# Kernel optimization log

Measured on AMD Instinct MI355X. Metric: run time of the kernel, lower is better.

Reference implementation:

```python
import jax, jax.numpy as jnp
import numpy as np

E = 1024          # n_embed_dim
H = 64            # head_size = n_embed_dim // n_heads (16)

def setup_inputs() -> dict:
    key = jax.random.key(0)
    k_x, k_q, k_k, k_v = jax.random.split(key, 4)
    scale = 1.0 / np.sqrt(E)
    return {
        "x": jax.random.normal(k_x, (4, 2048, E), dtype=jnp.float32),
        "ln_gamma": jnp.ones((E,), jnp.float32),
        "ln_beta": jnp.zeros((E,), jnp.float32),
        # torch nn.Linear weights: [out_features, in_features]
        "Wq": jax.random.normal(k_q, (H, E), dtype=jnp.float32) * scale,
        "Wk": jax.random.normal(k_k, (H, E), dtype=jnp.float32) * scale,
        "Wv": jax.random.normal(k_v, (H, E), dtype=jnp.float32) * scale,
    }

def reference(x, ln_gamma, ln_beta, Wq, Wk, Wv):
    # LayerNorm over last dim (eps matches torch default 1e-5)
    mu = jnp.mean(x, axis=-1, keepdims=True)
    var = jnp.mean(jnp.square(x - mu), axis=-1, keepdims=True)
    xn = (x - mu) * jax.lax.rsqrt(var + 1e-5) * ln_gamma + ln_beta

    q = jnp.einsum('bse,he->bsh', xn, Wq)   # [B,S,H]
    k = jnp.einsum('bse,he->bsh', xn, Wk)
    v = jnp.einsum('bse,he->bsh', xn, Wv)

    scores = jnp.einsum('bqh,bkh->bqk', q, k) / jnp.sqrt(jnp.float32(H))
    S = x.shape[1]
    causal = jnp.tril(jnp.ones((S, S), dtype=bool))
    scores = jnp.where(causal, scores, -jnp.inf)
    attn = jax.nn.softmax(scores, axis=-1)
    return jnp.einsum('bqk,bkh->bqh', attn, v)
```

## Files before the change

kernel.cpp:

```cpp
#include <hip/hip_runtime.h>

#define E 1024
#define HH 64
#define BB 4
#define SS 2048
#define BS (BB*SS)
#define NSLOT 144

typedef unsigned short u16;
typedef short bf16x8 __attribute__((ext_vector_type(8)));
typedef float f32x4 __attribute__((ext_vector_type(4)));

#define LOG2E_O8 0.18033688011112042f

__device__ inline u16 f2bf(float f) {
    unsigned int u = __float_as_uint(f);
    unsigned int r = (u + 0x7FFFu + ((u >> 16) & 1u)) >> 16;
    return (u16)r;
}

__global__ __launch_bounds__(256) void ln_kernel(const float* __restrict__ x,
        const float* __restrict__ gamma, const float* __restrict__ beta,
        u16* __restrict__ xn) {
    const int w = threadIdx.x >> 6, lane = threadIdx.x & 63;
    const size_t row = (size_t)blockIdx.x * 4 + w;
    const float4* xr = (const float4*)(x + row * E);
    float4 v[4];
    #pragma unroll
    for (int i = 0; i < 4; ++i) v[i] = xr[lane + 64 * i];
    float s = 0.f, sq = 0.f;
    #pragma unroll
    for (int i = 0; i < 4; ++i) {
        s  += v[i].x + v[i].y + v[i].z + v[i].w;
        sq += v[i].x*v[i].x + v[i].y*v[i].y + v[i].z*v[i].z + v[i].w*v[i].w;
    }
    #pragma unroll
    for (int off = 32; off > 0; off >>= 1) {
        s  += __shfl_xor(s,  off);
        sq += __shfl_xor(sq, off);
    }
    const float mean = s * (1.0f / E);
    const float var  = sq * (1.0f / E) - mean * mean;
    const float rstd = rsqrtf(var + 1e-5f);
    const float4* gr = (const float4*)gamma;
    const float4* br = (const float4*)beta;
    #pragma unroll
    for (int i = 0; i < 4; ++i) {
        const float4 g  = gr[lane + 64 * i];
        const float4 bt = br[lane + 64 * i];
        ushort4 o;
        o.x = f2bf((v[i].x - mean) * rstd * g.x + bt.x);
        o.y = f2bf((v[i].y - mean) * rstd * g.y + bt.y);
        o.z = f2bf((v[i].z - mean) * rstd * g.z + bt.z);
        o.w = f2bf((v[i].w - mean) * rstd * g.w + bt.w);
        *(ushort4*)(xn + row * E + (lane + 64 * i) * 4) = o;
    }
}

__global__ __launch_bounds__(256) void w_cast(const float* __restrict__ Wq,
        const float* __restrict__ Wk, const float* __restrict__ Wv,
        u16* __restrict__ wc) {
    const int row = blockIdx.x;
    const int t = threadIdx.x;
    const float* src = (row < 64)  ? (Wq + (size_t)row * E)
                     : (row < 128) ? (Wk + (size_t)(row - 64) * E)
                                   : (Wv + (size_t)(row - 128) * E);
    const float sc = (row < 64) ? LOG2E_O8 : 1.0f;
    const float4 v = *(const float4*)(src + t * 4);
    ushort4 o;
    o.x = f2bf(v.x * sc); o.y = f2bf(v.y * sc);
    o.z = f2bf(v.z * sc); o.w = f2bf(v.w * sc);
    *(ushort4*)(wc + (size_t)row * E + t * 4) = o;
}

__global__ __launch_bounds__(256) void qkv_mfma(const u16* __restrict__ xn,
        const u16* __restrict__ wc,
        u16* __restrict__ qb, u16* __restrict__ kb, u16* __restrict__ vt) {
    const int row0 = blockIdx.x * 32;
    const int t = threadIdx.x;
    const int w = t >> 6, lane = t & 63;
    const int quad = lane >> 4, r15 = lane & 15;
    __shared__ u16 Xs[32 * 64];
    __shared__ u16 Ws[192 * 64];
    f32x4 acc[2][3] = {};

    for (int kc = 0; kc < E; kc += 64) {
        __syncthreads();
        {
            const int row = t >> 3, ch = t & 7;
            const uint4 d = *(const uint4*)(xn + (size_t)(row0 + row) * E + kc + ch * 8);
            *(uint4*)&Xs[row * 64 + (ch ^ (row & 7)) * 8] = d;
        }
        #pragma unroll
        for (int i = 0; i < 6; ++i) {
            const int idx = i * 256 + t;
            const int wrow = idx >> 3, ch = idx & 7;
            const uint4 d = *(const uint4*)(wc + (size_t)wrow * E + kc + ch * 8);
            *(uint4*)&Ws[wrow * 64 + (ch ^ (wrow & 7)) * 8] = d;
        }
        __syncthreads();
        #pragma unroll
        for (int kk = 0; kk < 2; ++kk) {
            bf16x8 af[2];
            #pragma unroll
            for (int mt = 0; mt < 2; ++mt) {
                const int xrow = mt * 16 + r15;
                af[mt] = *(const bf16x8*)&Xs[xrow * 64 + ((kk * 4 + quad) ^ (xrow & 7)) * 8];
            }
            #pragma unroll
            for (int j = 0; j < 3; ++j) {
                const int wrow = (w * 3 + j) * 16 + r15;
                const bf16x8 bfr = *(const bf16x8*)&Ws[wrow * 64 + ((kk * 4 + quad) ^ (wrow & 7)) * 8];
                #pragma unroll
                for (int mt = 0; mt < 2; ++mt)
                    acc[mt][j] = __builtin_amdgcn_mfma_f32_16x16x32_bf16(af[mt], bfr, acc[mt][j], 0, 0, 0);
            }
        }
    }
    const int b    = row0 >> 11;
    const int key0 = row0 & 2047;
    #pragma unroll
    for (int mt = 0; mt < 2; ++mt)
        #pragma unroll
        for (int j = 0; j < 3; ++j) {
            const int cg  = w * 48 + j * 16 + r15;
            const int sel = cg >> 6;
            const int col = cg & 63;
            if (sel < 2) {
                u16* base = (sel == 0) ? qb : kb;
                #pragma unroll
                for (int r = 0; r < 4; ++r) {
                    const size_t row = (size_t)row0 + mt * 16 + quad * 4 + r;
                    base[row * HH + col] = f2bf(acc[mt][j][r]);
                }
            } else {
                ushort4 pk;
                pk.x = f2bf(acc[mt][j][0]); pk.y = f2bf(acc[mt][j][1]);
                pk.z = f2bf(acc[mt][j][2]); pk.w = f2bf(acc[mt][j][3]);
                *(ushort4*)(vt + (size_t)b * HH * SS + (size_t)col * SS
                               + key0 + mt * 16 + quad * 4) = pk;
            }
        }
}

__global__ __launch_bounds__(256) void attn_partial(const u16* __restrict__ qb,
        const u16* __restrict__ kb, const u16* __restrict__ vt,
        float* __restrict__ po, float* __restrict__ pm, float* __restrict__ pl) {
    const int bid = blockIdx.x;
    const int b   = bid >> 8;
    const int rem = bid & 255;
    const int qt  = rem >> 3, c = rem & 7;
    const int a   = qt >> 2;
    if (c > a) return;
    const int r_   = qt & 3;
    const int slot = b * NSLOT + 2 * a * (a + 1) + r_ * (a + 1) + c;
    const int q0   = qt << 6;
    const int t = threadIdx.x;
    const int w = t >> 6, lane = t & 63;
    const int quad = lane >> 4, r15 = lane & 15;

    __shared__ u16 Ks[64 * 64];
    __shared__ u16 VT[64 * 64];
    __shared__ u16 Ps[64 * 64];

    const size_t qrow = ((size_t)b * SS + q0 + w * 16 + r15) * HH;
    const bf16x8 qf0 = *(const bf16x8*)(qb + qrow + quad * 8);
    const bf16x8 qf1 = *(const bf16x8*)(qb + qrow + 32 + quad * 8);

    f32x4 o[4] = {};
    float m_[4], l_[4];
    #pragma unroll
    for (int r = 0; r < 4; ++r) { m_[r] = -INFINITY; l_[r] = 0.f; }

    const int t1 = min(c * 4 + 4, qt + 1);
    for (int tile = c * 4; tile < t1; ++tile) {
        const int kt = tile << 6;
        __syncthreads();
        {
            const int row = t >> 2, ch0 = (t & 3) * 2;
            const uint4* src = (const uint4*)(kb + ((size_t)b * SS + kt + row) * HH + ch0 * 8);
            const uint4 d0 = src[0], d1 = src[1];
            *(uint4*)&Ks[row * 64 + ((ch0    ) ^ (row & 7)) * 8] = d0;
            *(uint4*)&Ks[row * 64 + ((ch0 + 1) ^ (row & 7)) * 8] = d1;
        }
        {
            const int h = t >> 2, ch0 = (t & 3) * 2;
            const uint4* src = (const uint4*)(vt + (size_t)b * HH * SS + (size_t)h * SS + kt + ch0 * 8);
            const uint4 d0 = src[0], d1 = src[1];
            *(uint4*)&VT[h * 64 + ((ch0    ) ^ (h & 7)) * 8] = d0;
            *(uint4*)&VT[h * 64 + ((ch0 + 1) ^ (h & 7)) * 8] = d1;
        }
        __syncthreads();

        f32x4 s[4] = {};
        #pragma unroll
        for (int nt = 0; nt < 4; ++nt) {
            const int krow = nt * 16 + r15;
            const bf16x8 k0 = *(const bf16x8*)&Ks[krow * 64 + ((    quad) ^ (krow & 7)) * 8];
            const bf16x8 k1 = *(const bf16x8*)&Ks[krow * 64 + ((4 + quad) ^ (krow & 7)) * 8];
            s[nt] = __builtin_amdgcn_mfma_f32_16x16x32_bf16(qf0, k0, s[nt], 0, 0, 0);
            s[nt] = __builtin_amdgcn_mfma_f32_16x16x32_bf16(qf1, k1, s[nt], 0, 0, 0);
        }
        if (tile == qt) {
            #pragma unroll
            for (int nt = 0; nt < 4; ++nt)
                #pragma unroll
                for (int r = 0; r < 4; ++r)
                    if (nt * 16 + r15 > w * 16 + quad * 4 + r) s[nt][r] = -INFINITY;
        }

        float p[4][4];
        #pragma unroll
        for (int r = 0; r < 4; ++r) {
            float mx = fmaxf(fmaxf(s[0][r], s[1][r]), fmaxf(s[2][r], s[3][r]));
            mx = fmaxf(mx, __shfl_xor(mx, 1));
            mx = fmaxf(mx, __shfl_xor(mx, 2));
            mx = fmaxf(mx, __shfl_xor(mx, 4));
            mx = fmaxf(mx, __shfl_xor(mx, 8));
            const float mn = fmaxf(m_[r], mx);
            const float alpha = __builtin_amdgcn_exp2f(m_[r] - mn);
            m_[r] = mn;
            float rs = 0.f;
            #pragma unroll
            for (int nt = 0; nt < 4; ++nt) {
                p[nt][r] = __builtin_amdgcn_exp2f(s[nt][r] - mn);
                rs += p[nt][r];
            }
            rs += __shfl_xor(rs, 1); rs += __shfl_xor(rs, 2);
            rs += __shfl_xor(rs, 4); rs += __shfl_xor(rs, 8);
            l_[r] = l_[r] * alpha + rs;
            #pragma unroll
            for (int ht = 0; ht < 4; ++ht) o[ht][r] *= alpha;
        }

        #pragma unroll
        for (int nt = 0; nt < 4; ++nt)
            #pragma unroll
            for (int r = 0; r < 4; ++r) {
                const int prow = w * 16 + quad * 4 + r;
                const int col  = nt * 16 + r15;
                Ps[prow * 64 + (((col >> 3) ^ (prow & 7)) * 8) + (col & 7)] = f2bf(p[nt][r]);
            }
        const int arow = w * 16 + r15;
        const bf16x8 pf0 = *(const bf16x8*)&Ps[arow * 64 + ((    quad) ^ (arow & 7)) * 8];
        const bf16x8 pf1 = *(const bf16x8*)&Ps[arow * 64 + ((4 + quad) ^ (arow & 7)) * 8];

        #pragma unroll
        for (int ht = 0; ht < 4; ++ht) {
            const int vrow = ht * 16 + r15;
            const bf16x8 v0 = *(const bf16x8*)&VT[vrow * 64 + ((    quad) ^ (vrow & 7)) * 8];
            const bf16x8 v1 = *(const bf16x8*)&VT[vrow * 64 + ((4 + quad) ^ (vrow & 7)) * 8];
            o[ht] = __builtin_amdgcn_mfma_f32_16x16x32_bf16(pf0, v0, o[ht], 0, 0, 0);
            o[ht] = __builtin_amdgcn_mfma_f32_16x16x32_bf16(pf1, v1, o[ht], 0, 0, 0);
        }
    }

    #pragma unroll
    for (int r = 0; r < 4; ++r) {
        const int q = w * 16 + quad * 4 + r;
        #pragma unroll
        for (int ht = 0; ht < 4; ++ht)
            po[(size_t)slot * 4096 + q * 64 + ht * 16 + r15] = o[ht][r];
        if (r15 == 0) {
            pm[slot * 64 + q] = m_[r];
            pl[slot * 64 + q] = l_[r];
        }
    }
}

__global__ __launch_bounds__(256) void attn_reduce(const float* __restrict__ po,
        const float* __restrict__ pm, const float* __restrict__ pl,
        float* __restrict__ out) {
    const int bid = blockIdx.x;
    const int b = bid >> 7, rem = bid & 127;
    const int qt = rem >> 2, qq = rem & 3;
    const int a = qt >> 2, r_ = qt & 3;
    const int nc = a + 1;
    const int sbase = b * NSLOT + 2 * a * (a + 1) + r_ * (a + 1);
    const int t = threadIdx.x;
    const int h = t & 63, qr = t >> 6;
    #pragma unroll
    for (int i = 0; i < 4; ++i) {
        const int q = qq * 16 + qr * 4 + i;
        float mstar = -INFINITY;
        for (int cidx = 0; cidx < nc; ++cidx)
            mstar = fmaxf(mstar, pm[(sbase + cidx) * 64 + q]);
        float osum = 0.f, lsum = 0.f;
        for (int cidx = 0; cidx < nc; ++cidx) {
            const float sc = __builtin_amdgcn_exp2f(pm[(sbase + cidx) * 64 + q] - mstar);
            osum += sc * po[(size_t)(sbase + cidx) * 4096 + q * 64 + h];
            lsum += sc * pl[(sbase + cidx) * 64 + q];
        }
        out[((size_t)b * SS + (qt << 6) + q) * HH + h] = osum / lsum;
    }
}

extern "C" void kernel_launch(void* const* d_in, const int* in_sizes, int n_in,
                              void* d_out, int out_size, void* d_ws, size_t ws_size,
                              hipStream_t stream) {
    const float* x     = (const float*)d_in[0];
    const float* gamma = (const float*)d_in[1];
    const float* beta  = (const float*)d_in[2];
    const float* Wq    = (const float*)d_in[3];
    const float* Wk    = (const float*)d_in[4];
    const float* Wv    = (const float*)d_in[5];
    float* out = (float*)d_out;

    u16* xn = (u16*)d_ws;
    u16* wc = (u16*)((char*)d_ws + (size_t)BS * E * 2);
    u16* qb = (u16*)((char*)d_ws + (size_t)BS * E * 2 + 393216);
    u16* kb = qb + (size_t)BS * HH;
    u16* vt = kb + (size_t)BS * HH;
    float* po = (float*)d_ws;
    float* pm = po + (size_t)BB * NSLOT * 4096;
    float* pl = pm + (size_t)BB * NSLOT * 64;

    ln_kernel   <<<BS / 4,     256, 0, stream>>>(x, gamma, beta, xn);
    w_cast      <<<192,        256, 0, stream>>>(Wq, Wk, Wv, wc);
    qkv_mfma    <<<BS / 32,    256, 0, stream>>>(xn, wc, qb, kb, vt);
    attn_partial<<<BB * 32 * 8, 256, 0, stream>>>(qb, kb, vt, po, pm, pl);
    attn_reduce <<<BB * 32 * 4, 256, 0, stream>>>(po, pm, pl, out);
}
```

Before: 144.2 us.

## Fuse LayerNorm into QKV projection by folding gamma/beta into weights and bias

Result: slower. 175.7 us (+21.9%).

```diff
diff --git a/kernel.cpp b/kernel.cpp
--- a/kernel.cpp
+++ b/kernel.cpp
@@ -19,47 +19,10 @@
     return (u16)r;
 }
 
-__global__ __launch_bounds__(256) void ln_kernel(const float* __restrict__ x,
-        const float* __restrict__ gamma, const float* __restrict__ beta,
-        u16* __restrict__ xn) {
-    const int w = threadIdx.x >> 6, lane = threadIdx.x & 63;
-    const size_t row = (size_t)blockIdx.x * 4 + w;
-    const float4* xr = (const float4*)(x + row * E);
-    float4 v[4];
-    #pragma unroll
-    for (int i = 0; i < 4; ++i) v[i] = xr[lane + 64 * i];
-    float s = 0.f, sq = 0.f;
-    #pragma unroll
-    for (int i = 0; i < 4; ++i) {
-        s  += v[i].x + v[i].y + v[i].z + v[i].w;
-        sq += v[i].x*v[i].x + v[i].y*v[i].y + v[i].z*v[i].z + v[i].w*v[i].w;
-    }
-    #pragma unroll
-    for (int off = 32; off > 0; off >>= 1) {
-        s  += __shfl_xor(s,  off);
-        sq += __shfl_xor(sq, off);
-    }
-    const float mean = s * (1.0f / E);
-    const float var  = sq * (1.0f / E) - mean * mean;
-    const float rstd = rsqrtf(var + 1e-5f);
-    const float4* gr = (const float4*)gamma;
-    const float4* br = (const float4*)beta;
-    #pragma unroll
-    for (int i = 0; i < 4; ++i) {
-        const float4 g  = gr[lane + 64 * i];
-        const float4 bt = br[lane + 64 * i];
-        ushort4 o;
-        o.x = f2bf((v[i].x - mean) * rstd * g.x + bt.x);
-        o.y = f2bf((v[i].y - mean) * rstd * g.y + bt.y);
-        o.z = f2bf((v[i].z - mean) * rstd * g.z + bt.z);
-        o.w = f2bf((v[i].w - mean) * rstd * g.w + bt.w);
-        *(ushort4*)(xn + row * E + (lane + 64 * i) * 4) = o;
-    }
-}
-
 __global__ __launch_bounds__(256) void w_cast(const float* __restrict__ Wq,
         const float* __restrict__ Wk, const float* __restrict__ Wv,
-        u16* __restrict__ wc) {
+        const float* __restrict__ gamma, const float* __restrict__ beta,
+        u16* __restrict__ wc, float* __restrict__ bias) {
     const int row = blockIdx.x;
     const int t = threadIdx.x;
     const float* src = (row < 64)  ? (Wq + (size_t)row * E)
@@ -67,30 +30,65 @@
                                    : (Wv + (size_t)(row - 128) * E);
     const float sc = (row < 64) ? LOG2E_O8 : 1.0f;
     const float4 v = *(const float4*)(src + t * 4);
+    const float4 g = *(const float4*)(gamma + t * 4);
+    const float4 b = *(const float4*)(beta + t * 4);
     ushort4 o;
-    o.x = f2bf(v.x * sc); o.y = f2bf(v.y * sc);
-    o.z = f2bf(v.z * sc); o.w = f2bf(v.w * sc);
+    o.x = f2bf(v.x * g.x * sc); o.y = f2bf(v.y * g.y * sc);
+    o.z = f2bf(v.z * g.z * sc); o.w = f2bf(v.w * g.w * sc);
     *(ushort4*)(wc + (size_t)row * E + t * 4) = o;
-}
-
-__global__ __launch_bounds__(256) void qkv_mfma(const u16* __restrict__ xn,
-        const u16* __restrict__ wc,
+
+    float s = (v.x * b.x + v.y * b.y + v.z * b.z + v.w * b.w) * sc;
+    #pragma unroll
+    for (int off = 32; off > 0; off >>= 1) s += __shfl_xor(s, off);
+    __shared__ float red[4];
+    if ((t & 63) == 0) red[t >> 6] = s;
+    __syncthreads();
+    if (t == 0) bias[row] = red[0] + red[1] + red[2] + red[3];
+}
+
+__global__ __launch_bounds__(256) void lnqkv(const float* __restrict__ x,
+        const u16* __restrict__ wc, const float* __restrict__ bias,
         u16* __restrict__ qb, u16* __restrict__ kb, u16* __restrict__ vt) {
     const int row0 = blockIdx.x * 32;
     const int t = threadIdx.x;
     const int w = t >> 6, lane = t & 63;
     const int quad = lane >> 4, r15 = lane & 15;
-    __shared__ u16 Xs[32 * 64];
     __shared__ u16 Ws[192 * 64];
+    __shared__ float smu[32], srs[32];
+
+    #pragma unroll 2
+    for (int i = 0; i < 8; ++i) {
+        const int r = w * 8 + i;
+        const float4* xr = (const float4*)(x + (size_t)(row0 + r) * E);
+        float s = 0.f, sq = 0.f;
+        #pragma unroll
+        for (int jj = 0; jj < 4; ++jj) {
+            const float4 v = xr[lane + 64 * jj];
+            s  += v.x + v.y + v.z + v.w;
+            sq += v.x*v.x + v.y*v.y + v.z*v.z + v.w*v.w;
+        }
+        #pragma unroll
+        for (int off = 32; off > 0; off >>= 1) {
+            s  += __shfl_xor(s,  off);
+            sq += __shfl_xor(sq, off);
+        }
+        if (lane == 0) {
+            const float mean = s * (1.0f / E);
+            const float var  = sq * (1.0f / E) - mean * mean;
+            smu[r] = mean;
+            srs[r] = rsqrtf(var + 1e-5f);
+        }
+    }
+
+    float bj[3];
+    #pragma unroll
+    for (int j = 0; j < 3; ++j) bj[j] = bias[w * 48 + j * 16 + r15];
+
     f32x4 acc[2][3] = {};
+    const float* xbase = x + (size_t)row0 * E;
 
     for (int kc = 0; kc < E; kc += 64) {
         __syncthreads();
-        {
-            const int row = t >> 3, ch = t & 7;
-            const uint4 d = *(const uint4*)(xn + (size_t)(row0 + row) * E + kc + ch * 8);
-            *(uint4*)&Xs[row * 64 + (ch ^ (row & 7)) * 8] = d;
-        }
         #pragma unroll
         for (int i = 0; i < 6; ++i) {
             const int idx = i * 256 + t;
@@ -104,8 +102,17 @@
             bf16x8 af[2];
             #pragma unroll
             for (int mt = 0; mt < 2; ++mt) {
-                const int xrow = mt * 16 + r15;
-                af[mt] = *(const bf16x8*)&Xs[xrow * 64 + ((kk * 4 + quad) ^ (xrow & 7)) * 8];
+                const int rl = mt * 16 + r15;
+                const float* src = xbase + (size_t)rl * E + kc + kk * 32 + quad * 8;
+                const float4 f0 = *(const float4*)src;
+                const float4 f1 = *(const float4*)(src + 4);
+                const float mu = smu[rl], rs = srs[rl];
+                u16 tmp[8];
+                tmp[0] = f2bf((f0.x - mu) * rs); tmp[1] = f2bf((f0.y - mu) * rs);
+                tmp[2] = f2bf((f0.z - mu) * rs); tmp[3] = f2bf((f0.w - mu) * rs);
+                tmp[4] = f2bf((f1.x - mu) * rs); tmp[5] = f2bf((f1.y - mu) * rs);
+                tmp[6] = f2bf((f1.z - mu) * rs); tmp[7] = f2bf((f1.w - mu) * rs);
+                af[mt] = *(const bf16x8*)tmp;
             }
             #pragma unroll
             for (int j = 0; j < 3; ++j) {
@@ -117,6 +124,7 @@
             }
         }
     }
+
     const int b    = row0 >> 11;
     const int key0 = row0 & 2047;
     #pragma unroll
@@ -131,12 +139,12 @@
                 #pragma unroll
                 for (int r = 0; r < 4; ++r) {
                     const size_t row = (size_t)row0 + mt * 16 + quad * 4 + r;
-                    base[row * HH + col] = f2bf(acc[mt][j][r]);
+                    base[row * HH + col] = f2bf(acc[mt][j][r] + bj[j]);
                 }
             } else {
                 ushort4 pk;
-                pk.x = f2bf(acc[mt][j][0]); pk.y = f2bf(acc[mt][j][1]);
-                pk.z = f2bf(acc[mt][j][2]); pk.w = f2bf(acc[mt][j][3]);
+                pk.x = f2bf(acc[mt][j][0] + bj[j]); pk.y = f2bf(acc[mt][j][1] + bj[j]);
+                pk.z = f2bf(acc[mt][j][2] + bj[j]); pk.w = f2bf(acc[mt][j][3] + bj[j]);
                 *(ushort4*)(vt + (size_t)b * HH * SS + (size_t)col * SS
                                + key0 + mt * 16 + quad * 4) = pk;
             }
@@ -306,18 +314,18 @@
     const float* Wv    = (const float*)d_in[5];
     float* out = (float*)d_out;
 
-    u16* xn = (u16*)d_ws;
-    u16* wc = (u16*)((char*)d_ws + (size_t)BS * E * 2);
-    u16* qb = (u16*)((char*)d_ws + (size_t)BS * E * 2 + 393216);
-    u16* kb = qb + (size_t)BS * HH;
-    u16* vt = kb + (size_t)BS * HH;
-    float* po = (float*)d_ws;
-    float* pm = po + (size_t)BB * NSLOT * 4096;
-    float* pl = pm + (size_t)BB * NSLOT * 64;
-
-    ln_kernel   <<<BS / 4,     256, 0, stream>>>(x, gamma, beta, xn);
-    w_cast      <<<192,        256, 0, stream>>>(Wq, Wk, Wv, wc);
-    qkv_mfma    <<<BS / 32,    256, 0, stream>>>(xn, wc, qb, kb, vt);
+    char* p = (char*)d_ws;
+    u16*   wc   = (u16*)p;                         p += 393216;
+    float* bias = (float*)p;                       p += 1024;
+    u16*   qb   = (u16*)p;                         p += (size_t)BS * HH * 2;
+    u16*   kb   = (u16*)p;                         p += (size_t)BS * HH * 2;
+    u16*   vt   = (u16*)p;                         p += (size_t)BS * HH * 2;
+    float* po   = (float*)p;                       p += (size_t)BB * NSLOT * 4096 * 4;
+    float* pm   = (float*)p;                       p += (size_t)BB * NSLOT * 64 * 4;
+    float* pl   = (float*)p;
+
+    w_cast      <<<192,         256, 0, stream>>>(Wq, Wk, Wv, gamma, beta, wc, bias);
+    lnqkv       <<<BS / 32,     256, 0, stream>>>(x, wc, bias, qb, kb, vt);
     attn_partial<<<BB * 32 * 8, 256, 0, stream>>>(qb, kb, vt, po, pm, pl);
     attn_reduce <<<BB * 32 * 4, 256, 0, stream>>>(po, pm, pl, out);
 }
```

## Fuse LN with weight cast, halve QKV tile, split attention into finer key chunks

Applied to the files above, without the earlier changes.

Result: slower. 154.7 us (+7.3%).

```diff
diff --git a/kernel.cpp b/kernel.cpp
--- a/kernel.cpp
+++ b/kernel.cpp
@@ -5,7 +5,7 @@
 #define BB 4
 #define SS 2048
 #define BS (BB*SS)
-#define NSLOT 144
+#define NSLOT 272
 
 typedef unsigned short u16;
 typedef short bf16x8 __attribute__((ext_vector_type(8)));
@@ -19,74 +19,76 @@
     return (u16)r;
 }
 
-__global__ __launch_bounds__(256) void ln_kernel(const float* __restrict__ x,
+__global__ __launch_bounds__(256) void ln_wcast(const float* __restrict__ x,
         const float* __restrict__ gamma, const float* __restrict__ beta,
-        u16* __restrict__ xn) {
-    const int w = threadIdx.x >> 6, lane = threadIdx.x & 63;
-    const size_t row = (size_t)blockIdx.x * 4 + w;
-    const float4* xr = (const float4*)(x + row * E);
-    float4 v[4];
-    #pragma unroll
-    for (int i = 0; i < 4; ++i) v[i] = xr[lane + 64 * i];
-    float s = 0.f, sq = 0.f;
-    #pragma unroll
-    for (int i = 0; i < 4; ++i) {
-        s  += v[i].x + v[i].y + v[i].z + v[i].w;
-        sq += v[i].x*v[i].x + v[i].y*v[i].y + v[i].z*v[i].z + v[i].w*v[i].w;
-    }
-    #pragma unroll
-    for (int off = 32; off > 0; off >>= 1) {
-        s  += __shfl_xor(s,  off);
-        sq += __shfl_xor(sq, off);
-    }
-    const float mean = s * (1.0f / E);
-    const float var  = sq * (1.0f / E) - mean * mean;
-    const float rstd = rsqrtf(var + 1e-5f);
-    const float4* gr = (const float4*)gamma;
-    const float4* br = (const float4*)beta;
-    #pragma unroll
-    for (int i = 0; i < 4; ++i) {
-        const float4 g  = gr[lane + 64 * i];
-        const float4 bt = br[lane + 64 * i];
+        const float* __restrict__ Wq, const float* __restrict__ Wk,
+        const float* __restrict__ Wv,
+        u16* __restrict__ xn, u16* __restrict__ wc, float* __restrict__ bias) {
+    __shared__ float red[4];
+    const int t = threadIdx.x;
+    if (blockIdx.x < 2048) {
+        const int w = t >> 6, lane = t & 63;
+        const size_t row = (size_t)blockIdx.x * 4 + w;
+        const float4* xr = (const float4*)(x + row * E);
+        float4 v[4];
+        #pragma unroll
+        for (int i = 0; i < 4; ++i) v[i] = xr[lane + 64 * i];
+        float s = 0.f, sq = 0.f;
+        #pragma unroll
+        for (int i = 0; i < 4; ++i) {
+            s  += v[i].x + v[i].y + v[i].z + v[i].w;
+            sq += v[i].x*v[i].x + v[i].y*v[i].y + v[i].z*v[i].z + v[i].w*v[i].w;
+        }
+        #pragma unroll
+        for (int off = 32; off > 0; off >>= 1) {
+            s  += __shfl_xor(s,  off);
+            sq += __shfl_xor(sq, off);
+        }
+        const float mean = s * (1.0f / E);
+        const float var  = sq * (1.0f / E) - mean * mean;
+        const float rstd = rsqrtf(var + 1e-5f);
+        const float4* gr = (const float4*)gamma;
+        const float4* br = (const float4*)beta;
+        #pragma unroll
+        for (int i = 0; i < 4; ++i) {
+            const float4 g  = gr[lane + 64 * i];
+            const float4 bt = br[lane + 64 * i];
+            ushort4 o;
+            o.x = f2bf((v[i].x - mean) * rstd * g.x + bt.x);
+            o.y = f2bf((v[i].y - mean) * rstd * g.y + bt.y);
+            o.z = f2bf((v[i].z - mean) * rstd * g.z + bt.z);
+            o.w = f2bf((v[i].w - mean) * rstd * g.w + bt.w);
+            *(ushort4*)(xn + row * E + (lane + 64 * i) * 4) = o;
+        }
+    } else {
+        const int row = blockIdx.x - 2048;
+        const float* src = (row < 64)  ? (Wq + (size_t)row * E)
+                         : (row < 128) ? (Wk + (size_t)(row - 64) * E)
+                                       : (Wv + (size_t)(row - 128) * E);
+        const float sc = (row < 64) ? LOG2E_O8 : 1.0f;
+        const float4 v = *(const float4*)(src + t * 4);
         ushort4 o;
-        o.x = f2bf((v[i].x - mean) * rstd * g.x + bt.x);
-        o.y = f2bf((v[i].y - mean) * rstd * g.y + bt.y);
-        o.z = f2bf((v[i].z - mean) * rstd * g.z + bt.z);
-        o.w = f2bf((v[i].w - mean) * rstd * g.w + bt.w);
-        *(ushort4*)(xn + row * E + (lane + 64 * i) * 4) = o;
-    }
-}
-
-__global__ __launch_bounds__(256) void w_cast(const float* __restrict__ Wq,
-        const float* __restrict__ Wk, const float* __restrict__ Wv,
-        u16* __restrict__ wc) {
-    const int row = blockIdx.x;
-    const int t = threadIdx.x;
-    const float* src = (row < 64)  ? (Wq + (size_t)row * E)
-                     : (row < 128) ? (Wk + (size_t)(row - 64) * E)
-                                   : (Wv + (size_t)(row - 128) * E);
-    const float sc = (row < 64) ? LOG2E_O8 : 1.0f;
-    const float4 v = *(const float4*)(src + t * 4);
-    ushort4 o;
-    o.x = f2bf(v.x * sc); o.y = f2bf(v.y * sc);
-    o.z = f2bf(v.z * sc); o.w = f2bf(v.w * sc);
-    *(ushort4*)(wc + (size_t)row * E + t * 4) = o;
+        o.x = f2bf(v.x * sc); o.y = f2bf(v.y * sc);
+        o.z = f2bf(v.z * sc); o.w = f2bf(v.w * sc);
+        *(ushort4*)(wc + (size_t)row * E + t * 4) = o;
+        (void)red; (void)bias;
+    }
 }
 
 __global__ __launch_bounds__(256) void qkv_mfma(const u16* __restrict__ xn,
         const u16* __restrict__ wc,
         u16* __restrict__ qb, u16* __restrict__ kb, u16* __restrict__ vt) {
-    const int row0 = blockIdx.x * 32;
+    const int row0 = blockIdx.x * 16;
     const int t = threadIdx.x;
     const int w = t >> 6, lane = t & 63;
     const int quad = lane >> 4, r15 = lane & 15;
-    __shared__ u16 Xs[32 * 64];
+    __shared__ u16 Xs[16 * 64];
     __shared__ u16 Ws[192 * 64];
-    f32x4 acc[2][3] = {};
+    f32x4 acc[3] = {};
 
     for (int kc = 0; kc < E; kc += 64) {
         __syncthreads();
-        {
+        if (t < 128) {
             const int row = t >> 3, ch = t & 7;
             const uint4 d = *(const uint4*)(xn + (size_t)(row0 + row) * E + kc + ch * 8);
             *(uint4*)&Xs[row * 64 + (ch ^ (row & 7)) * 8] = d;
@@ -101,59 +103,49 @@
         __syncthreads();
         #pragma unroll
         for (int kk = 0; kk < 2; ++kk) {
-            bf16x8 af[2];
-            #pragma unroll
-            for (int mt = 0; mt < 2; ++mt) {
-                const int xrow = mt * 16 + r15;
-                af[mt] = *(const bf16x8*)&Xs[xrow * 64 + ((kk * 4 + quad) ^ (xrow & 7)) * 8];
-            }
+            const bf16x8 af = *(const bf16x8*)&Xs[r15 * 64 + ((kk * 4 + quad) ^ (r15 & 7)) * 8];
             #pragma unroll
             for (int j = 0; j < 3; ++j) {
                 const int wrow = (w * 3 + j) * 16 + r15;
                 const bf16x8 bfr = *(const bf16x8*)&Ws[wrow * 64 + ((kk * 4 + quad) ^ (wrow & 7)) * 8];
-                #pragma unroll
-                for (int mt = 0; mt < 2; ++mt)
-                    acc[mt][j] = __builtin_amdgcn_mfma_f32_16x16x32_bf16(af[mt], bfr, acc[mt][j], 0, 0, 0);
+                acc[j] = __builtin_amdgcn_mfma_f32_16x16x32_bf16(af, bfr, acc[j], 0, 0, 0);
             }
         }
     }
     const int b    = row0 >> 11;
     const int key0 = row0 & 2047;
     #pragma unroll
-    for (int mt = 0; mt < 2; ++mt)
-        #pragma unroll
-        for (int j = 0; j < 3; ++j) {
-            const int cg  = w * 48 + j * 16 + r15;
-            const int sel = cg >> 6;
-            const int col = cg & 63;
-            if (sel < 2) {
-                u16* base = (sel == 0) ? qb : kb;
-                #pragma unroll
-                for (int r = 0; r < 4; ++r) {
-                    const size_t row = (size_t)row0 + mt * 16 + quad * 4 + r;
-                    base[row * HH + col] = f2bf(acc[mt][j][r]);
-                }
-            } else {
-                ushort4 pk;
-                pk.x = f2bf(acc[mt][j][0]); pk.y = f2bf(acc[mt][j][1]);
-                pk.z = f2bf(acc[mt][j][2]); pk.w = f2bf(acc[mt][j][3]);
-                *(ushort4*)(vt + (size_t)b * HH * SS + (size_t)col * SS
-                               + key0 + mt * 16 + quad * 4) = pk;
+    for (int j = 0; j < 3; ++j) {
+        const int cg  = w * 48 + j * 16 + r15;
+        const int sel = cg >> 6;
+        const int col = cg & 63;
+        if (sel < 2) {
+            u16* base = (sel == 0) ? qb : kb;
+            #pragma unroll
+            for (int r = 0; r < 4; ++r) {
+                const size_t row = (size_t)row0 + quad * 4 + r;
+                base[row * HH + col] = f2bf(acc[j][r]);
             }
-        }
+        } else {
+            ushort4 pk;
+            pk.x = f2bf(acc[j][0]); pk.y = f2bf(acc[j][1]);
+            pk.z = f2bf(acc[j][2]); pk.w = f2bf(acc[j][3]);
+            *(ushort4*)(vt + (size_t)b * HH * SS + (size_t)col * SS + key0 + quad * 4) = pk;
+        }
+    }
 }
 
 __global__ __launch_bounds__(256) void attn_partial(const u16* __restrict__ qb,
         const u16* __restrict__ kb, const u16* __restrict__ vt,
-        float* __restrict__ po, float* __restrict__ pm, float* __restrict__ pl) {
+        float* __restrict__ po, float* __restrict__ pm, float* __restrict__ pl,
+        float* __restrict__ out) {
     const int bid = blockIdx.x;
-    const int b   = bid >> 8;
-    const int rem = bid & 255;
-    const int qt  = rem >> 3, c = rem & 7;
-    const int a   = qt >> 2;
-    if (c > a) return;
-    const int r_   = qt & 3;
-    const int slot = b * NSLOT + 2 * a * (a + 1) + r_ * (a + 1) + c;
+    const int b   = bid >> 9;
+    const int rem = bid & 511;
+    const int qt  = rem >> 4, c = rem & 15;
+    if (c > (qt >> 1)) return;
+    const int nc   = (qt >> 1) + 1;
+    const int slot = b * NSLOT + (((qt + 1) * (qt + 1)) >> 2) + c;
     const int q0   = qt << 6;
     const int t = threadIdx.x;
     const int w = t >> 6, lane = t & 63;
@@ -172,8 +164,8 @@
     #pragma unroll
     for (int r = 0; r < 4; ++r) { m_[r] = -INFINITY; l_[r] = 0.f; }
 
-    const int t1 = min(c * 4 + 4, qt + 1);
-    for (int tile = c * 4; tile < t1; ++tile) {
+    const int t1 = min(c * 2 + 2, qt + 1);
+    for (int tile = c * 2; tile < t1; ++tile) {
         const int kt = tile << 6;
         __syncthreads();
         {
@@ -255,6 +247,17 @@
         }
     }
 
+    if (nc == 1) {
+        #pragma unroll
+        for (int r = 0; r < 4; ++r) {
+            const float inv = 1.0f / l_[r];
+            const size_t orow = ((size_t)b * SS + q0 + w * 16 + quad * 4 + r) * HH;
+            #pragma unroll
+            for (int ht = 0; ht < 4; ++ht)
+                out[orow + ht * 16 + r15] = o[ht][r] * inv;
+        }
+        return;
+    }
     #pragma unroll
     for (int r = 0; r < 4; ++r) {
         const int q = w * 16 + quad * 4 + r;
@@ -274,9 +277,9 @@
     const int bid = blockIdx.x;
     const int b = bid >> 7, rem = bid & 127;
     const int qt = rem >> 2, qq = rem & 3;
-    const int a = qt >> 2, r_ = qt & 3;
-    const int nc = a + 1;
-    const int sbase = b * NSLOT + 2 * a * (a + 1) + r_ * (a + 1);
+    if (qt < 2) return;
+    const int nc = (qt >> 1) + 1;
+    const int sbase = b * NSLOT + (((qt + 1) * (qt + 1)) >> 2);
     const int t = threadIdx.x;
     const int h = t & 63, qr = t >> 6;
     #pragma unroll
@@ -306,18 +309,19 @@
     const float* Wv    = (const float*)d_in[5];
     float* out = (float*)d_out;
 
-    u16* xn = (u16*)d_ws;
-    u16* wc = (u16*)((char*)d_ws + (size_t)BS * E * 2);
-    u16* qb = (u16*)((char*)d_ws + (size_t)BS * E * 2 + 393216);
-    u16* kb = qb + (size_t)BS * HH;
-    u16* vt = kb + (size_t)BS * HH;
-    float* po = (float*)d_ws;
-    float* pm = po + (size_t)BB * NSLOT * 4096;
-    float* pl = pm + (size_t)BB * NSLOT * 64;
-
-    ln_kernel   <<<BS / 4,     256, 0, stream>>>(x, gamma, beta, xn);
-    w_cast      <<<192,        256, 0, stream>>>(Wq, Wk, Wv, wc);
-    qkv_mfma    <<<BS / 32,    256, 0, stream>>>(xn, wc, qb, kb, vt);
-    attn_partial<<<BB * 32 * 8, 256, 0, stream>>>(qb, kb, vt, po, pm, pl);
-    attn_reduce <<<BB * 32 * 4, 256, 0, stream>>>(po, pm, pl, out);
-}
+    char* p = (char*)d_ws;
+    u16*   xn   = (u16*)p;                         p += (size_t)BS * E * 2;
+    u16*   wc   = (u16*)p;                         p += 393216;
+    float* bias = (float*)p;                       p += 1024;
+    u16*   qb   = (u16*)p;                         p += (size_t)BS * HH * 2;
+    u16*   kb   = (u16*)p;                         p += (size_t)BS * HH * 2;
+    u16*   vt   = (u16*)p;                         p += (size_t)BS * HH * 2;
+    float* po   = (float*)p;                       p += (size_t)BB * NSLOT * 4096 * 4;
+    float* pm   = (float*)p;                       p += (size_t)BB * NSLOT * 64 * 4;
+    float* pl   = (float*)p;
+
+    ln_wcast    <<<2048 + 192,   256, 0, stream>>>(x, gamma, beta, Wq, Wk, Wv, xn, wc, bias);
+    qkv_mfma    <<<BS / 16,      256, 0, stream>>>(xn, wc, qb, kb, vt);
+    attn_partial<<<BB * 32 * 16, 256, 0, stream>>>(qb, kb, vt, po, pm, pl, out);
+    attn_reduce <<<BB * 32 * 4,  256, 0, stream>>>(po, pm, pl, out);
+}
```
